# Kernel tuning notes

Hardware: AMD Instinct MI355X
Metric: run time of the kernel (lower is better)

The kernel has to match this reference:

```python
import jax, jax.numpy as jnp
import numpy as np

B, S, D = 1, 2048, 4096
NH, NKV, HD = 32, 8, 128
REP = NH // NKV
HID = 14336
MAXS = 4096
THETA = 1e6
EPS = 1e-5
NEG = -1e9


def setup_inputs() -> dict:
    key = jax.random.key(0)
    ks = jax.random.split(key, 16)
    s = 0.02
    inp = {
        'x': jax.random.normal(ks[0], (B, S, D), jnp.float32),
        'cache': jnp.zeros((2, 1, B, NKV, MAXS, HD), jnp.float32),
        'wq': jax.random.normal(ks[1], (NH * HD, D), jnp.float32) * s,
        'bq': jax.random.normal(ks[2], (NH * HD,), jnp.float32) * s,
        'wk': jax.random.normal(ks[3], (NKV * HD, D), jnp.float32) * s,
        'bk': jax.random.normal(ks[4], (NKV * HD,), jnp.float32) * s,
        'wv': jax.random.normal(ks[5], (NKV * HD, D), jnp.float32) * s,
        'bv': jax.random.normal(ks[6], (NKV * HD,), jnp.float32) * s,
        'wo': jax.random.normal(ks[7], (D, NH * HD), jnp.float32) * s,
        'w_gate': jax.random.normal(ks[8], (HID, D), jnp.float32) * s,
        'w_up': jax.random.normal(ks[9], (HID, D), jnp.float32) * s,
        'w_down': jax.random.normal(ks[10], (D, HID), jnp.float32) * s,
        'ln1_w': jnp.ones((D,), jnp.float32),
        'ln2_w': jnp.ones((D,), jnp.float32),
        'storage_idx': jnp.arange(S, dtype=jnp.int32),
    }
    return inp


def _rmsnorm(x, w):
    xf = x.astype(jnp.float32)
    n = xf * jax.lax.rsqrt(jnp.mean(xf * xf, axis=-1, keepdims=True) + EPS)
    return n.astype(x.dtype) * w


def _rope_tables():
    inv_freq = 1.0 / (THETA ** (jnp.arange(0, HD, 2, dtype=jnp.float32) / HD))
    t = jnp.arange(MAXS, dtype=jnp.float32)
    freqs = jnp.outer(t, inv_freq)              # [MAXS, HD/2]
    emb = jnp.concatenate([freqs, freqs], -1)   # [MAXS, HD]
    return jnp.cos(emb), jnp.sin(emb)


def _rotate_half(x):
    x1, x2 = x[..., : HD // 2], x[..., HD // 2:]
    return jnp.concatenate([-x2, x1], axis=-1)


def reference(x, cache, wq, bq, wk, bk, wv, bv, wo, w_gate, w_up, w_down,
              ln1_w, ln2_w, storage_idx):
    h_in = _rmsnorm(x, ln1_w)
    xq = (h_in @ wq.T + bq).reshape(B, S, NH, HD).transpose(0, 2, 1, 3)   # [B,NH,S,HD]
    xk = (h_in @ wk.T + bk).reshape(B, S, NKV, HD).transpose(0, 2, 1, 3)  # [B,NKV,S,HD]
    xv = (h_in @ wv.T + bv).reshape(B, S, NKV, HD).transpose(0, 2, 1, 3)

    cos, sin = _rope_tables()
    cos_p = cos[storage_idx][None, None]  # [1,1,S,HD]
    sin_p = sin[storage_idx][None, None]
    xq = xq * cos_p + _rotate_half(xq) * sin_p
    xk = xk * cos_p + _rotate_half(xk) * sin_p

    # KV-cache index_copy along the sequence dim
    keys = cache[0, 0].at[:, :, storage_idx, :].set(xk)    # [B,NKV,MAXS,HD]
    values = cache[1, 0].at[:, :, storage_idx, :].set(xv)

    # causal additive mask, rows indexed by storage positions
    pos = jnp.arange(MAXS)
    mask = jnp.where(pos[None, :] <= storage_idx[:, None], 0.0, NEG)  # [S,MAXS]

    # GQA attention without materializing repeated KV heads
    xq_g = xq.reshape(B, NKV, REP, S, HD)
    scores = jnp.einsum('bgrsd,bgtd->bgrst', xq_g, keys) / jnp.sqrt(jnp.float32(HD))
    scores = scores + mask  # broadcast over [B,NKV,REP]
    attn = jax.nn.softmax(scores, axis=-1)
    out = jnp.einsum('bgrst,bgtd->bgrsd', attn, values)
    out = out.reshape(B, NH, S, HD).transpose(0, 2, 1, 3).reshape(B, S, NH * HD)
    h = out @ wo.T

    r = x + h
    h2 = _rmsnorm(r, ln2_w)
    ffn = (jax.nn.silu(h2 @ w_gate.T) * (h2 @ w_up.T)) @ w_down.T
    return r + ffn
```

## Files before the change

### kernel.cpp

```cpp
#include <hip/hip_runtime.h>
#include <cstddef>

typedef __bf16 v8bf __attribute__((ext_vector_type(8)));
typedef __bf16 v4bf __attribute__((ext_vector_type(4)));
typedef float  v4f  __attribute__((ext_vector_type(4)));

#define S_LEN 2048
#define D_DIM 4096
#define NH    32
#define NKV   8
#define HD    128

__device__ inline v4f mfma16(v8bf a, v8bf b, v4f c) {
    return __builtin_amdgcn_mfma_f32_16x16x32_bf16(a, b, c, 0, 0, 0);
}

__global__ __launch_bounds__(256) void rmsnorm_bf16(
    const float* __restrict__ x, const float* __restrict__ w, __bf16* __restrict__ out)
{
    const int D = D_DIM;
    int row = blockIdx.x;
    const float4* xr = (const float4*)(x + (size_t)row * D);
    const float4* wr = (const float4*)w;
    int tid = threadIdx.x;
    float4 v[4];
    float ss = 0.f;
#pragma unroll
    for (int i = 0; i < 4; i++) {
        v[i] = xr[tid + i * 256];
        ss += v[i].x * v[i].x + v[i].y * v[i].y + v[i].z * v[i].z + v[i].w * v[i].w;
    }
#pragma unroll
    for (int off = 32; off; off >>= 1) ss += __shfl_xor(ss, off);
    __shared__ float red[4];
    if ((tid & 63) == 0) red[tid >> 6] = ss;
    __syncthreads();
    ss = red[0] + red[1] + red[2] + red[3];
    float rs = rsqrtf(ss * (1.f / D) + 1e-5f);
#pragma unroll
    for (int i = 0; i < 4; i++) {
        float4 ww = wr[tid + i * 256];
        v4bf t;
        t[0] = (__bf16)(v[i].x * rs * ww.x);
        t[1] = (__bf16)(v[i].y * rs * ww.y);
        t[2] = (__bf16)(v[i].z * rs * ww.z);
        t[3] = (__bf16)(v[i].w * rs * ww.w);
        *(v4bf*)&out[(size_t)row * D + (size_t)(tid + i * 256) * 4] = t;
    }
}

template <typename OutT, bool HAS_BIAS, bool HAS_RES>
__global__ __launch_bounds__(256) void gemm_bt(
    const __bf16* __restrict__ A, const float* __restrict__ W,
    const float* __restrict__ bias, const float* res, OutT* C, int N, int K)
{
    constexpr int BK = 64;
    __shared__ __align__(16) __bf16 As[128 * BK];
    __shared__ __align__(16) __bf16 Ws[128 * BK];
    int m0 = blockIdx.y * 128, n0 = blockIdx.x * 128;
    int tid = threadIdx.x;
    int w = tid >> 6, l = tid & 63, g = l >> 4, c = l & 15;
    int wm = (w >> 1) * 64, wn = (w & 1) * 64;
    v4f zero = {0.f, 0.f, 0.f, 0.f};
    v4f acc[4][4];
#pragma unroll
    for (int i = 0; i < 4; i++)
#pragma unroll
        for (int j = 0; j < 4; j++) acc[i][j] = zero;

    for (int k0 = 0; k0 < K; k0 += BK) {
        __syncthreads();
#pragma unroll
        for (int i = 0; i < 4; i++) {
            int ch = tid + i * 256;
            int r = ch >> 3, c8 = ch & 7;
            *(uint4*)&As[r * BK + c8 * 8] =
                *(const uint4*)&A[(size_t)(m0 + r) * K + k0 + c8 * 8];
        }
#pragma unroll
        for (int i = 0; i < 8; i++) {
            int ch = tid + i * 256;
            int r = ch >> 4, c4 = ch & 15;
            float4 f = *(const float4*)&W[(size_t)(n0 + r) * K + k0 + c4 * 4];
            v4bf t;
            t[0] = (__bf16)f.x; t[1] = (__bf16)f.y; t[2] = (__bf16)f.z; t[3] = (__bf16)f.w;
            *(v4bf*)&Ws[r * BK + c4 * 4] = t;
        }
        __syncthreads();
#pragma unroll
        for (int kk = 0; kk < BK; kk += 32) {
            v8bf af[4], wf[4];
#pragma unroll
            for (int i = 0; i < 4; i++) af[i] = *(const v8bf*)&As[(wm + i * 16 + c) * BK + kk + g * 8];
#pragma unroll
            for (int j = 0; j < 4; j++) wf[j] = *(const v8bf*)&Ws[(wn + j * 16 + c) * BK + kk + g * 8];
#pragma unroll
            for (int i = 0; i < 4; i++)
#pragma unroll
                for (int j = 0; j < 4; j++) acc[i][j] = mfma16(af[i], wf[j], acc[i][j]);
        }
    }
#pragma unroll
    for (int i = 0; i < 4; i++)
#pragma unroll
        for (int j = 0; j < 4; j++) {
            int mm = m0 + wm + i * 16 + g * 4;
            int nn = n0 + wn + j * 16 + c;
#pragma unroll
            for (int r = 0; r < 4; r++) {
                float vv = acc[i][j][r];
                if (HAS_BIAS) vv += bias[nn];
                if (HAS_RES) vv += res[(size_t)(mm + r) * N + nn];
                C[(size_t)(mm + r) * N + nn] = (OutT)vv;
            }
        }
}

__global__ __launch_bounds__(256) void rope_inplace(
    __bf16* Q, __bf16* K, const int* __restrict__ sidx)
{
    int s = blockIdx.x;
    float p = (float)sidx[s];
    for (int t = threadIdx.x; t < (NH + NKV) * 64; t += 256) {
        int head = t >> 6, d = t & 63;
        float inv = __expf(-0.2158673520f * (float)d);
        float sn, cs;
        sincosf(p * inv, &sn, &cs);
        __bf16* base;
        if (head < NH) base = Q + ((size_t)s * NH + head) * HD + d;
        else           base = K + ((size_t)s * NKV + (head - NH)) * HD + d;
        float x1 = (float)base[0], x2 = (float)base[64];
        base[0]  = (__bf16)(x1 * cs - x2 * sn);
        base[64] = (__bf16)(x2 * cs + x1 * sn);
    }
}

__device__ inline int kswz(int key, int col8) {
    return key * 128 + (col8 ^ ((key & 7) << 3));
}
__device__ inline int vswz(int feat) {
    return ((feat ^ (feat >> 3)) & 7) << 3;
}

__global__ __launch_bounds__(256) void flash_attn(
    const __bf16* __restrict__ Q, const __bf16* __restrict__ K,
    const __bf16* __restrict__ V, __bf16* __restrict__ O)
{
    const float scale = 0.08838834764831845f;
    const int NQT = S_LEN / 64;
    int bx = blockIdx.x, h = blockIdx.y;
    int kvh = h >> 2;
    int tid = threadIdx.x;
    int w = tid >> 6, l = tid & 63, g = l >> 4, c = l & 15;

    __shared__ __align__(16) __bf16 Ks[32 * 128];
    __shared__ __align__(16) __bf16 Vt[128 * 64];
    __shared__ __align__(16) __bf16 Pl[4][16][40];

    for (int pass = 0; pass < 2; ++pass) {
        int qt = pass ? (NQT - 1 - bx) : bx;
        int q0 = qt * 64;
        int rowbase = q0 + w * 16;

        v8bf qf[4];
#pragma unroll
        for (int kk = 0; kk < 4; kk++)
            qf[kk] = *(const v8bf*)&Q[((size_t)(rowbase + c) * NH + h) * HD + kk * 32 + g * 8];

        float m_r[4], l_r[4], alpha[4];
        v4f zero = {0.f, 0.f, 0.f, 0.f};
        v4f o[8];
#pragma unroll
        for (int f = 0; f < 8; f++) o[f] = zero;
#pragma unroll
        for (int r = 0; r < 4; r++) { m_r[r] = -1e30f; l_r[r] = 0.f; }

        int ntiles = 2 * qt + 2;
        for (int t = 0; t < ntiles; t++) {
            int j0 = t * 32;
            __syncthreads();
#pragma unroll
            for (int i = 0; i < 2; i++) {
                int ch = tid + i * 256;
                int key = ch >> 4, f8 = ch & 15;
                size_t gidx = ((size_t)(j0 + key) * NKV + kvh) * HD + f8 * 8;
                *(uint4*)&Ks[kswz(key, f8 * 8)] = *(const uint4*)&K[gidx];
                v8bf vv = *(const v8bf*)&V[gidx];
#pragma unroll
                for (int j = 0; j < 8; j++) {
                    int feat = f8 * 8 + j;
                    Vt[feat * 64 + (key ^ vswz(feat))] = vv[j];
                }
            }
            __syncthreads();
            v4f s0 = zero, s1 = zero;
            __builtin_amdgcn_s_setprio(1);
#pragma unroll
            for (int kk = 0; kk < 4; kk++) {
                v8bf k0f = *(const v8bf*)&Ks[kswz(c, kk * 32 + g * 8)];
                v8bf k1f = *(const v8bf*)&Ks[kswz(16 + c, kk * 32 + g * 8)];
                s0 = mfma16(qf[kk], k0f, s0);
                s1 = mfma16(qf[kk], k1f, s1);
            }
            __builtin_amdgcn_s_setprio(0);
            float p0[4], p1[4];
#pragma unroll
            for (int r = 0; r < 4; r++) {
                int row = rowbase + g * 4 + r;
                float a = s0[r] * scale, b = s1[r] * scale;
                if (j0 + c > row) a = -1e30f;
                if (j0 + 16 + c > row) b = -1e30f;
                float v = fmaxf(a, b);
                v = fmaxf(v, __shfl_xor(v, 1));
                v = fmaxf(v, __shfl_xor(v, 2));
                v = fmaxf(v, __shfl_xor(v, 4));
                v = fmaxf(v, __shfl_xor(v, 8));
                float mn = fmaxf(m_r[r], v);
                float al = __expf(m_r[r] - mn);
                float e0 = __expf(a - mn), e1 = __expf(b - mn);
                float srow = e0 + e1;
                srow += __shfl_xor(srow, 1);
                srow += __shfl_xor(srow, 2);
                srow += __shfl_xor(srow, 4);
                srow += __shfl_xor(srow, 8);
                l_r[r] = al * l_r[r] + srow;
                m_r[r] = mn;
                alpha[r] = al;
                p0[r] = e0; p1[r] = e1;
            }
#pragma unroll
            for (int f = 0; f < 8; f++)
#pragma unroll
                for (int r = 0; r < 4; r++) o[f][r] *= alpha[r];
#pragma unroll
            for (int r = 0; r < 4; r++) {
                Pl[w][g * 4 + r][c] = (__bf16)p0[r];
                Pl[w][g * 4 + r][16 + c] = (__bf16)p1[r];
            }
            __syncthreads();
            v8bf pf = *(const v8bf*)&Pl[w][c][g * 8];
            __builtin_amdgcn_s_setprio(1);
#pragma unroll
            for (int f = 0; f < 8; f++) {
                int feat = f * 16 + c;
                v8bf vf = *(const v8bf*)&Vt[feat * 64 + ((g * 8) ^ vswz(feat))];
                o[f] = mfma16(pf, vf, o[f]);
            }
            __builtin_amdgcn_s_setprio(0);
        }
#pragma unroll
        for (int f = 0; f < 8; f++)
#pragma unroll
            for (int r = 0; r < 4; r++) {
                float val = o[f][r] / l_r[r];
                O[((size_t)(rowbase + g * 4 + r) * NH + h) * HD + f * 16 + c] = (__bf16)val;
            }
    }
}

__global__ __launch_bounds__(256) void silu_mul(
    const __bf16* __restrict__ g, const __bf16* __restrict__ u, __bf16* __restrict__ out)
{
    size_t i = ((size_t)blockIdx.x * 256 + threadIdx.x) * 8;
    v8bf gv = *(const v8bf*)&g[i];
    v8bf uv = *(const v8bf*)&u[i];
    v8bf ov;
#pragma unroll
    for (int j = 0; j < 8; j++) {
        float x = (float)gv[j];
        float s = x / (1.f + __expf(-x));
        ov[j] = (__bf16)(s * (float)uv[j]);
    }
    *(v8bf*)&out[i] = ov;
}

extern "C" void kernel_launch(void* const* d_in, const int* in_sizes, int n_in,
                              void* d_out, int out_size, void* d_ws, size_t ws_size,
                              hipStream_t stream)
{
    const float* x   = (const float*)d_in[0];
    const float* wq  = (const float*)d_in[2];
    const float* bq  = (const float*)d_in[3];
    const float* wk  = (const float*)d_in[4];
    const float* bk  = (const float*)d_in[5];
    const float* wv  = (const float*)d_in[6];
    const float* bv  = (const float*)d_in[7];
    const float* wo  = (const float*)d_in[8];
    const float* wg  = (const float*)d_in[9];
    const float* wu  = (const float*)d_in[10];
    const float* wd  = (const float*)d_in[11];
    const float* ln1 = (const float*)d_in[12];
    const float* ln2 = (const float*)d_in[13];
    const int* sidx  = (const int*)d_in[14];
    float* out = (float*)d_out;

    char* ws = (char*)d_ws;
    const size_t MB = 1u << 20;
    __bf16* h_in = (__bf16*)(ws + 0 * MB);
    __bf16* q_b  = (__bf16*)(ws + 16 * MB);
    __bf16* k_b  = (__bf16*)(ws + 32 * MB);
    __bf16* v_b  = (__bf16*)(ws + 36 * MB);
    __bf16* ao   = (__bf16*)(ws + 40 * MB);
    __bf16* h2   = (__bf16*)(ws + 56 * MB);
    __bf16* gate = (__bf16*)(ws + 72 * MB);
    __bf16* up   = (__bf16*)(ws + 128 * MB);
    __bf16* mid  = (__bf16*)(ws + 184 * MB);

    rmsnorm_bf16<<<S_LEN, 256, 0, stream>>>(x, ln1, h_in);
    gemm_bt<__bf16, true, false><<<dim3(32, 16), 256, 0, stream>>>(h_in, wq, bq, nullptr, q_b, 4096, 4096);
    gemm_bt<__bf16, true, false><<<dim3(8, 16), 256, 0, stream>>>(h_in, wk, bk, nullptr, k_b, 1024, 4096);
    gemm_bt<__bf16, true, false><<<dim3(8, 16), 256, 0, stream>>>(h_in, wv, bv, nullptr, v_b, 1024, 4096);
    rope_inplace<<<S_LEN, 256, 0, stream>>>(q_b, k_b, sidx);
    flash_attn<<<dim3(S_LEN / 128, NH), 256, 0, stream>>>(q_b, k_b, v_b, ao);
    gemm_bt<float, false, true><<<dim3(32, 16), 256, 0, stream>>>(ao, wo, nullptr, x, out, 4096, 4096);
    rmsnorm_bf16<<<S_LEN, 256, 0, stream>>>(out, ln2, h2);
    gemm_bt<__bf16, false, false><<<dim3(112, 16), 256, 0, stream>>>(h2, wg, nullptr, nullptr, gate, 14336, 4096);
    gemm_bt<__bf16, false, false><<<dim3(112, 16), 256, 0, stream>>>(h2, wu, nullptr, nullptr, up, 14336, 4096);
    silu_mul<<<(S_LEN * 14336) / (256 * 8), 256, 0, stream>>>(gate, up, mid);
    gemm_bt<float, false, true><<<dim3(32, 16), 256, 0, stream>>>(mid, wd, nullptr, out, out, 4096, 14336);
}
```

Baseline: 2.641 ms.

## Pre-convert weights to bf16, use direct-to-LDS loads with swizzle, fuse SiLU-mul into up GEMM

When the workspace is large enough, all fp32 weights are converted to bf16 in separate kernels each call, and the GEMMs then load A and W tiles straight into LDS with global_load_lds using an XOR swizzle to avoid bank conflicts. The SiLU-gate multiply moves into the up-projection epilogue, which drops the separate silu_mul kernel and the up buffer. Blocks are remapped across the grid in groups of eight for better L2 locality. The conversion pass adds an extra read and write of every weight per call, which competes with the savings from halving weight traffic inside the GEMMs.

```diff
diff --git a/kernel.cpp b/kernel.cpp
--- a/kernel.cpp
+++ b/kernel.cpp
@@ -13,6 +13,24 @@
 
 __device__ inline v4f mfma16(v8bf a, v8bf b, v4f c) {
     return __builtin_amdgcn_mfma_f32_16x16x32_bf16(a, b, c, 0, 0, 0);
+}
+
+__device__ inline void gload16(const void* g, void* l) {
+    __builtin_amdgcn_global_load_lds(
+        (const __attribute__((address_space(1))) void*)g,
+        (__attribute__((address_space(3))) void*)l, 16, 0, 0);
+}
+
+__global__ __launch_bounds__(256) void f32_to_bf16(
+    const float* __restrict__ src, __bf16* __restrict__ dst, int n4)
+{
+    int stride = gridDim.x * 256;
+    for (int i = blockIdx.x * 256 + threadIdx.x; i < n4; i += stride) {
+        float4 f = ((const float4*)src)[i];
+        v4bf t;
+        t[0] = (__bf16)f.x; t[1] = (__bf16)f.y; t[2] = (__bf16)f.z; t[3] = (__bf16)f.w;
+        ((v4bf*)dst)[i] = t;
+    }
 }
 
 __global__ __launch_bounds__(256) void rmsnorm_bf16(
@@ -49,18 +67,30 @@
     }
 }
 
-template <typename OutT, bool HAS_BIAS, bool HAS_RES>
+template <typename OutT, bool W_BF16, bool HAS_BIAS, bool HAS_RES, bool HAS_GLU>
 __global__ __launch_bounds__(256) void gemm_bt(
-    const __bf16* __restrict__ A, const float* __restrict__ W,
-    const float* __restrict__ bias, const float* res, OutT* C, int N, int K)
+    const __bf16* __restrict__ A, const void* __restrict__ Wp,
+    const float* __restrict__ bias, const float* __restrict__ res,
+    const __bf16* __restrict__ glu, OutT* __restrict__ C, int N, int K)
 {
     constexpr int BK = 64;
     __shared__ __align__(16) __bf16 As[128 * BK];
     __shared__ __align__(16) __bf16 Ws[128 * BK];
-    int m0 = blockIdx.y * 128, n0 = blockIdx.x * 128;
+
+    int nwg = gridDim.x * gridDim.y;
+    int bid = blockIdx.y * gridDim.x + blockIdx.x;
+    int cpx = nwg >> 3;
+    int sbid = (bid & 7) * cpx + (bid >> 3);
+    int m0 = (sbid / gridDim.x) * 128, n0 = (sbid % gridDim.x) * 128;
+
     int tid = threadIdx.x;
     int w = tid >> 6, l = tid & 63, g = l >> 4, c = l & 15;
     int wm = (w >> 1) * 64, wn = (w & 1) * 64;
+
+    int srow = tid >> 3;
+    int sj   = tid & 7;
+    int sjj  = sj ^ (srow & 7);
+
     v4f zero = {0.f, 0.f, 0.f, 0.f};
     v4f acc[4][4];
 #pragma unroll
@@ -72,28 +102,46 @@
         __syncthreads();
 #pragma unroll
         for (int i = 0; i < 4; i++) {
-            int ch = tid + i * 256;
-            int r = ch >> 3, c8 = ch & 7;
-            *(uint4*)&As[r * BK + c8 * 8] =
-                *(const uint4*)&A[(size_t)(m0 + r) * K + k0 + c8 * 8];
-        }
-#pragma unroll
-        for (int i = 0; i < 8; i++) {
-            int ch = tid + i * 256;
-            int r = ch >> 4, c4 = ch & 15;
-            float4 f = *(const float4*)&W[(size_t)(n0 + r) * K + k0 + c4 * 4];
-            v4bf t;
-            t[0] = (__bf16)f.x; t[1] = (__bf16)f.y; t[2] = (__bf16)f.z; t[3] = (__bf16)f.w;
-            *(v4bf*)&Ws[r * BK + c4 * 4] = t;
+            int r = i * 32 + srow;
+            gload16(&A[(size_t)(m0 + r) * K + k0 + sjj * 8],
+                    (char*)As + r * 128 + sj * 16);
+        }
+        if (W_BF16) {
+            const __bf16* W = (const __bf16*)Wp;
+#pragma unroll
+            for (int i = 0; i < 4; i++) {
+                int r = i * 32 + srow;
+                gload16(&W[(size_t)(n0 + r) * K + k0 + sjj * 8],
+                        (char*)Ws + r * 128 + sj * 16);
+            }
+        } else {
+            const float* W = (const float*)Wp;
+#pragma unroll
+            for (int i = 0; i < 8; i++) {
+                int ch = tid + i * 256;
+                int r = ch >> 4, c4 = ch & 15;
+                float4 f = *(const float4*)&W[(size_t)(n0 + r) * K + k0 + c4 * 4];
+                v4bf t;
+                t[0] = (__bf16)f.x; t[1] = (__bf16)f.y; t[2] = (__bf16)f.z; t[3] = (__bf16)f.w;
+                int phys = r * 128 + (((c4 >> 1) ^ (r & 7)) << 4) + ((c4 & 1) << 3);
+                *(v4bf*)((char*)Ws + phys) = t;
+            }
         }
         __syncthreads();
 #pragma unroll
         for (int kk = 0; kk < BK; kk += 32) {
+            int jb = kk >> 3;
             v8bf af[4], wf[4];
 #pragma unroll
-            for (int i = 0; i < 4; i++) af[i] = *(const v8bf*)&As[(wm + i * 16 + c) * BK + kk + g * 8];
-#pragma unroll
-            for (int j = 0; j < 4; j++) wf[j] = *(const v8bf*)&Ws[(wn + j * 16 + c) * BK + kk + g * 8];
+            for (int i = 0; i < 4; i++) {
+                int row = wm + i * 16 + c;
+                af[i] = *(const v8bf*)((char*)As + row * 128 + (((jb + g) ^ (c & 7)) << 4));
+            }
+#pragma unroll
+            for (int j = 0; j < 4; j++) {
+                int row = wn + j * 16 + c;
+                wf[j] = *(const v8bf*)((char*)Ws + row * 128 + (((jb + g) ^ (c & 7)) << 4));
+            }
 #pragma unroll
             for (int i = 0; i < 4; i++)
 #pragma unroll
@@ -111,6 +159,10 @@
                 float vv = acc[i][j][r];
                 if (HAS_BIAS) vv += bias[nn];
                 if (HAS_RES) vv += res[(size_t)(mm + r) * N + nn];
+                if (HAS_GLU) {
+                    float gx = (float)glu[(size_t)(mm + r) * N + nn];
+                    vv *= gx / (1.f + __expf(-gx));
+                }
                 C[(size_t)(mm + r) * N + nn] = (OutT)vv;
             }
         }
@@ -258,22 +310,6 @@
     }
 }
 
-__global__ __launch_bounds__(256) void silu_mul(
-    const __bf16* __restrict__ g, const __bf16* __restrict__ u, __bf16* __restrict__ out)
-{
-    size_t i = ((size_t)blockIdx.x * 256 + threadIdx.x) * 8;
-    v8bf gv = *(const v8bf*)&g[i];
-    v8bf uv = *(const v8bf*)&u[i];
-    v8bf ov;
-#pragma unroll
-    for (int j = 0; j < 8; j++) {
-        float x = (float)gv[j];
-        float s = x / (1.f + __expf(-x));
-        ov[j] = (__bf16)(s * (float)uv[j]);
-    }
-    *(v8bf*)&out[i] = ov;
-}
-
 extern "C" void kernel_launch(void* const* d_in, const int* in_sizes, int n_in,
                               void* d_out, int out_size, void* d_ws, size_t ws_size,
                               hipStream_t stream)
@@ -295,7 +331,7 @@
     float* out = (float*)d_out;
 
     char* ws = (char*)d_ws;
-    const size_t MB = 1u << 20;
+    const size_t MB = 1ull << 20;
     __bf16* h_in = (__bf16*)(ws + 0 * MB);
     __bf16* q_b  = (__bf16*)(ws + 16 * MB);
     __bf16* k_b  = (__bf16*)(ws + 32 * MB);
@@ -303,19 +339,49 @@
     __bf16* ao   = (__bf16*)(ws + 40 * MB);
     __bf16* h2   = (__bf16*)(ws + 56 * MB);
     __bf16* gate = (__bf16*)(ws + 72 * MB);
-    __bf16* up   = (__bf16*)(ws + 128 * MB);
-    __bf16* mid  = (__bf16*)(ws + 184 * MB);
-
-    rmsnorm_bf16<<<S_LEN, 256, 0, stream>>>(x, ln1, h_in);
-    gemm_bt<__bf16, true, false><<<dim3(32, 16), 256, 0, stream>>>(h_in, wq, bq, nullptr, q_b, 4096, 4096);
-    gemm_bt<__bf16, true, false><<<dim3(8, 16), 256, 0, stream>>>(h_in, wk, bk, nullptr, k_b, 1024, 4096);
-    gemm_bt<__bf16, true, false><<<dim3(8, 16), 256, 0, stream>>>(h_in, wv, bv, nullptr, v_b, 1024, 4096);
-    rope_inplace<<<S_LEN, 256, 0, stream>>>(q_b, k_b, sidx);
-    flash_attn<<<dim3(S_LEN / 128, NH), 256, 0, stream>>>(q_b, k_b, v_b, ao);
-    gemm_bt<float, false, true><<<dim3(32, 16), 256, 0, stream>>>(ao, wo, nullptr, x, out, 4096, 4096);
-    rmsnorm_bf16<<<S_LEN, 256, 0, stream>>>(out, ln2, h2);
-    gemm_bt<__bf16, false, false><<<dim3(112, 16), 256, 0, stream>>>(h2, wg, nullptr, nullptr, gate, 14336, 4096);
-    gemm_bt<__bf16, false, false><<<dim3(112, 16), 256, 0, stream>>>(h2, wu, nullptr, nullptr, up, 14336, 4096);
-    silu_mul<<<(S_LEN * 14336) / (256 * 8), 256, 0, stream>>>(gate, up, mid);
-    gemm_bt<float, false, true><<<dim3(32, 16), 256, 0, stream>>>(mid, wd, nullptr, out, out, 4096, 14336);
-}
+    __bf16* mid  = (__bf16*)(ws + 128 * MB);
+
+    bool big = ws_size >= 600 * MB;
+
+    if (big) {
+        __bf16* wq_b = (__bf16*)(ws + 184 * MB);
+        __bf16* wk_b = (__bf16*)(ws + 216 * MB);
+        __bf16* wv_b = (__bf16*)(ws + 224 * MB);
+        __bf16* wo_b = (__bf16*)(ws + 232 * MB);
+        __bf16* wg_b = (__bf16*)(ws + 264 * MB);
+        __bf16* wu_b = (__bf16*)(ws + 376 * MB);
+        __bf16* wd_b = (__bf16*)(ws + 488 * MB);
+
+        f32_to_bf16<<<2048, 256, 0, stream>>>(wq, wq_b, (D_DIM * D_DIM) / 4);
+        f32_to_bf16<<<2048, 256, 0, stream>>>(wk, wk_b, (1024 * D_DIM) / 4);
+        f32_to_bf16<<<2048, 256, 0, stream>>>(wv, wv_b, (1024 * D_DIM) / 4);
+        f32_to_bf16<<<2048, 256, 0, stream>>>(wo, wo_b, (D_DIM * D_DIM) / 4);
+        f32_to_bf16<<<2048, 256, 0, stream>>>(wg, wg_b, (14336 * D_DIM) / 4);
+        f32_to_bf16<<<2048, 256, 0, stream>>>(wu, wu_b, (14336 * D_DIM) / 4);
+        f32_to_bf16<<<2048, 256, 0, stream>>>(wd, wd_b, (D_DIM * 14336) / 4);
+
+        rmsnorm_bf16<<<S_LEN, 256, 0, stream>>>(x, ln1, h_in);
+        gemm_bt<__bf16, true, true, false, false><<<dim3(32, 16), 256, 0, stream>>>(h_in, wq_b, bq, nullptr, nullptr, q_b, 4096, 4096);
+        gemm_bt<__bf16, true, true, false, false><<<dim3(8, 16), 256, 0, stream>>>(h_in, wk_b, bk, nullptr, nullptr, k_b, 1024, 4096);
+        gemm_bt<__bf16, true, true, false, false><<<dim3(8, 16), 256, 0, stream>>>(h_in, wv_b, bv, nullptr, nullptr, v_b, 1024, 4096);
+        rope_inplace<<<S_LEN, 256, 0, stream>>>(q_b, k_b, sidx);
+        flash_attn<<<dim3(S_LEN / 128, NH), 256, 0, stream>>>(q_b, k_b, v_b, ao);
+        gemm_bt<float, true, false, true, false><<<dim3(32, 16), 256, 0, stream>>>(ao, wo_b, nullptr, x, nullptr, out, 4096, 4096);
+        rmsnorm_bf16<<<S_LEN, 256, 0, stream>>>(out, ln2, h2);
+        gemm_bt<__bf16, true, false, false, false><<<dim3(112, 16), 256, 0, stream>>>(h2, wg_b, nullptr, nullptr, nullptr, gate, 14336, 4096);
+        gemm_bt<__bf16, true, false, false, true><<<dim3(112, 16), 256, 0, stream>>>(h2, wu_b, nullptr, nullptr, gate, mid, 14336, 4096);
+        gemm_bt<float, true, false, true, false><<<dim3(32, 16), 256, 0, stream>>>(mid, wd_b, nullptr, out, nullptr, out, 4096, 14336);
+    } else {
+        rmsnorm_bf16<<<S_LEN, 256, 0, stream>>>(x, ln1, h_in);
+        gemm_bt<__bf16, false, true, false, false><<<dim3(32, 16), 256, 0, stream>>>(h_in, wq, bq, nullptr, nullptr, q_b, 4096, 4096);
+        gemm_bt<__bf16, false, true, false, false><<<dim3(8, 16), 256, 0, stream>>>(h_in, wk, bk, nullptr, nullptr, k_b, 1024, 4096);
+        gemm_bt<__bf16, false, true, false, false><<<dim3(8, 16), 256, 0, stream>>>(h_in, wv, bv, nullptr, nullptr, v_b, 1024, 4096);
+        rope_inplace<<<S_LEN, 256, 0, stream>>>(q_b, k_b, sidx);
+        flash_attn<<<dim3(S_LEN / 128, NH), 256, 0, stream>>>(q_b, k_b, v_b, ao);
+        gemm_bt<float, false, false, true, false><<<dim3(32, 16), 256, 0, stream>>>(ao, wo, nullptr, x, nullptr, out, 4096, 4096);
+        rmsnorm_bf16<<<S_LEN, 256, 0, stream>>>(out, ln2, h2);
+        gemm_bt<__bf16, false, false, false, false><<<dim3(112, 16), 256, 0, stream>>>(h2, wg, nullptr, nullptr, nullptr, gate, 14336, 4096);
+        gemm_bt<__bf16, false, false, false, true><<<dim3(112, 16), 256, 0, stream>>>(h2, wu, nullptr, nullptr, gate, mid, 14336, 4096);
+        gemm_bt<float, false, false, true, false><<<dim3(32, 16), 256, 0, stream>>>(mid, wd, nullptr, out, nullptr, out, 4096, 14336);
+    }
+}
```

Result: faster. 2.305 ms (-12.7%).
